# Kernel optimization log

Measured on AMD Instinct MI355X. Metric: run time of the kernel, lower is better.

The kernel has to match this reference:

```python
import jax, jax.numpy as jnp
import numpy as np

N, E, IN_D, H, OUT_D = 50000, 800000, 128, 64, 64


def setup_inputs() -> dict:
    key = jax.random.key(0)
    ks = jax.random.split(key, 16)
    s = lambda k, shape: jax.random.normal(k, shape, dtype=jnp.float32) * (1.0 / np.sqrt(shape[0]))
    return {
        "x": jax.random.normal(ks[0], (N, IN_D), dtype=jnp.float32),
        "edge_index": jax.random.randint(ks[1], (2, E), 0, N, dtype=jnp.int32),
        "W1": s(ks[2], (IN_D, H)), "b1": jnp.zeros((H,), jnp.float32),
        "W2": s(ks[3], (H, 2 * H)), "b2": jnp.zeros((2 * H,), jnp.float32),
        "W3": s(ks[4], (2 * H, 4 * H)), "b3": jnp.zeros((4 * H,), jnp.float32),
        "dec1_w": s(ks[5], (4 * H, 2 * H, 2)), "dec1_b": jnp.zeros((2 * H,), jnp.float32),
        "dec2_w": s(ks[6], (2 * H, H, 2)), "dec2_b": jnp.zeros((H,), jnp.float32),
        "dec3_w": s(ks[7], (H, H, 2)), "dec3_b": jnp.zeros((H,), jnp.float32),
        "skip1_w": s(ks[8], (2 * H, 2 * H)), "skip1_b": jnp.zeros((2 * H,), jnp.float32),
        "skip2_w": s(ks[9], (H, H)), "skip2_b": jnp.zeros((H,), jnp.float32),
        "fin_w": s(ks[10], (OUT_D, 8 * H)), "fin_b": jnp.zeros((OUT_D,), jnp.float32),
    }


def _deconv2(x, w, b):
    # ConvTranspose1d(kernel=2, stride=2): [n,c,l] x [c,o,2] -> [n,o,2l]
    y = jnp.einsum('ncl,cok->nolk', x, w)
    n, o = x.shape[0], w.shape[1]
    return y.reshape(n, o, -1) + b[None, :, None]


def reference(x, edge_index, W1, b1, W2, b2, W3, b3, dec1_w, dec1_b, dec2_w, dec2_b,
              dec3_w, dec3_b, skip1_w, skip1_b, skip2_w, skip2_b, fin_w, fin_b):
    n = x.shape[0]
    loop = jnp.arange(n, dtype=edge_index.dtype)
    src = jnp.concatenate([edge_index[0], loop])
    tgt = jnp.concatenate([edge_index[1], loop])
    deg = jax.ops.segment_sum(jnp.ones_like(src, dtype=x.dtype), tgt, num_segments=n)
    dinv = jax.lax.rsqrt(deg)  # deg >= 1 due to self-loops
    norm = dinv[src] * dinv[tgt]  # [E+N]

    def gcn(h, W, b):
        hw = h @ W
        agg = jax.ops.segment_sum(hw[src] * norm[:, None], tgt, num_segments=n)
        return agg + b

    x1 = jax.nn.gelu(gcn(x, W1, b1))    # [N, H]
    x2 = jax.nn.gelu(gcn(x1, W2, b2))   # [N, 2H]
    x3 = jax.nn.gelu(gcn(x2, W3, b3))   # [N, 4H]

    d = _deconv2(x3[:, :, None], dec1_w, dec1_b)           # [N, 2H, 2]
    d = d + (x2 @ skip1_w.T + skip1_b)[:, :, None]
    d = _deconv2(d, dec2_w, dec2_b)                        # [N, H, 4]
    d = d + (x1 @ skip2_w.T + skip2_b)[:, :, None]
    d = _deconv2(d, dec3_w, dec3_b)                        # [N, H, 8]
    out = d.reshape(n, -1) @ fin_w.T + fin_b               # [N, OUT_D]
    return out
```

## Files before the change

### kernel.cpp

```cpp
#include <hip/hip_runtime.h>
#include <hip/hip_bf16.h>

typedef __attribute__((ext_vector_type(8))) short short8_t;
typedef __attribute__((ext_vector_type(4))) float f32x4;

#define CAP 64

__device__ __forceinline__ float gelu_f(float x) {
    float x3 = x * x * x;
    return 0.5f * x * (1.0f + tanhf(0.7978845608028654f * (x + 0.044715f * x3)));
}
__device__ __forceinline__ float b2f(unsigned short u) {
    union { float f; unsigned int i; } c; c.i = ((unsigned int)u) << 16; return c.f;
}
__device__ __forceinline__ unsigned short f2bu(float f) {
    union { float f; unsigned int i; } c; c.f = f;
    unsigned int r = c.i + 0x7fffu + ((c.i >> 16) & 1u);
    return (unsigned short)(r >> 16);
}


__device__ __forceinline__ void d_EF(int bid, int t, const float* __restrict__ dec3_w,
                                     const float* __restrict__ fin_w, float* __restrict__ EF) {
    int i2 = bid * 4 + (t >> 6), od = t & 63;
    int c3 = i2 >> 2, pp = i2 & 3;
    const float* d3 = dec3_w + c3 * 128;
    const float* fw = fin_w + od * 512;
    float s = 0.f;
    #pragma unroll
    for (int o3 = 0; o3 < 64; ++o3) {
        s += d3[o3 * 2 + 0] * fw[o3 * 8 + pp * 2 + 0];
        s += d3[o3 * 2 + 1] * fw[o3 * 8 + pp * 2 + 1];
    }
    EF[i2 * 64 + od] = s;
}

__device__ __forceinline__ void d_CEF(int bid, int t, const float* __restrict__ dec2_w,
                                      const float* __restrict__ EF, float* __restrict__ CEF) {
    int i1 = bid * 4 + (t >> 6), od = t & 63;
    int c2 = i1 >> 1, lp = i1 & 1;
    const float* d2 = dec2_w + c2 * 128;
    float s = 0.f;
    #pragma unroll
    for (int o2 = 0; o2 < 64; ++o2) {
        s += d2[o2 * 2 + 0] * EF[(o2 * 4 + lp * 2 + 0) * 64 + od];
        s += d2[o2 * 2 + 1] * EF[(o2 * 4 + lp * 2 + 1) * 64 + od];
    }
    CEF[i1 * 64 + od] = s;
}

__device__ __forceinline__ void d_comp(int sb, int od,
                       const float* __restrict__ dec1_w, const float* __restrict__ skip1_w,
                       const float* __restrict__ skip2_w,
                       const float* __restrict__ dec1_b, const float* __restrict__ skip1_b,
                       const float* __restrict__ dec2_b, const float* __restrict__ skip2_b,
                       const float* __restrict__ dec3_b, const float* __restrict__ fin_w,
                       const float* __restrict__ fin_b,
                       const float* __restrict__ CEF, const float* __restrict__ EF,
                       unsigned short* __restrict__ McatT, float* __restrict__ m0) {
    if (sb < 256) {
        const float* d1 = dec1_w + sb * 256;
        float s = 0.f;
        for (int j = 0; j < 256; ++j) s += d1[j] * CEF[j * 64 + od];
        McatT[od * 448 + sb] = f2bu(s);
    } else if (sb < 384) {
        int c = sb - 256;
        float s = 0.f;
        for (int j = 0; j < 256; ++j) s += skip1_w[(j >> 1) * 128 + c] * CEF[j * 64 + od];
        McatT[od * 448 + sb] = f2bu(s);
    } else if (sb < 448) {
        int c = sb - 384;
        float s = 0.f;
        for (int j = 0; j < 256; ++j) s += skip2_w[(j >> 2) * 64 + c] * EF[j * 64 + od];
        McatT[od * 448 + sb] = f2bu(s);
    } else {
        float s = fin_b[od];
        for (int j = 0; j < 256; ++j) s += (dec1_b[j >> 1] + skip1_b[j >> 1]) * CEF[j * 64 + od];
        for (int j = 0; j < 256; ++j) s += (dec2_b[j >> 2] + skip2_b[j >> 2]) * EF[j * 64 + od];
        for (int j = 0; j < 512; ++j) s += dec3_b[j >> 3] * fin_w[od * 512 + j];
        m0[od] = s;
    }
}

__device__ __forceinline__ void d_wconv(int bid, int t,
                        const float* __restrict__ W1, const float* __restrict__ W2,
                        const float* __restrict__ W3,
                        unsigned short* __restrict__ W1T, unsigned short* __restrict__ W2T,
                        unsigned short* __restrict__ W3T) {
    int i = bid * 256 + t;
    if (i < 8192) {
        int k = i >> 6, n = i & 63;
        W1T[n * 128 + k] = f2bu(W1[i]);
    } else if (i < 16384) {
        int j = i - 8192; int k = j >> 7, n = j & 127;
        W2T[n * 64 + k] = f2bu(W2[j]);
    } else if (i < 49152) {
        int j = i - 16384; int k = j >> 8, n = j & 255;
        W3T[n * 128 + k] = f2bu(W3[j]);
    }
}

__device__ __forceinline__ void d_fillx(int bid, int t, const int* __restrict__ src,
                                        const int* __restrict__ tgt, int E,
                                        int* __restrict__ cnt, unsigned short* __restrict__ csru) {
    int i = (bid * 256 + t) * 8;
    if (i + 7 < E) {
        int4 t0 = *(const int4*)(tgt + i);
        int4 t1 = *(const int4*)(tgt + i + 4);
        int4 s0 = *(const int4*)(src + i);
        int4 s1 = *(const int4*)(src + i + 4);
        int k0 = atomicAdd(&cnt[t0.x], 1);
        int k1 = atomicAdd(&cnt[t0.y], 1);
        int k2 = atomicAdd(&cnt[t0.z], 1);
        int k3 = atomicAdd(&cnt[t0.w], 1);
        int k4 = atomicAdd(&cnt[t1.x], 1);
        int k5 = atomicAdd(&cnt[t1.y], 1);
        int k6 = atomicAdd(&cnt[t1.z], 1);
        int k7 = atomicAdd(&cnt[t1.w], 1);
        if (k0 < CAP - 1) csru[(t0.x << 6) + k0] = (unsigned short)s0.x;
        if (k1 < CAP - 1) csru[(t0.y << 6) + k1] = (unsigned short)s0.y;
        if (k2 < CAP - 1) csru[(t0.z << 6) + k2] = (unsigned short)s0.z;
        if (k3 < CAP - 1) csru[(t0.w << 6) + k3] = (unsigned short)s0.w;
        if (k4 < CAP - 1) csru[(t1.x << 6) + k4] = (unsigned short)s1.x;
        if (k5 < CAP - 1) csru[(t1.y << 6) + k5] = (unsigned short)s1.y;
        if (k6 < CAP - 1) csru[(t1.z << 6) + k6] = (unsigned short)s1.z;
        if (k7 < CAP - 1) csru[(t1.w << 6) + k7] = (unsigned short)s1.w;
    } else {
        for (int k = i; k < E; ++k) {
            int tt = tgt[k];
            int kk = atomicAdd(&cnt[tt], 1);
            if (kk < CAP - 1) csru[(tt << 6) + kk] = (unsigned short)src[k];
        }
    }
}

template<bool A32, bool BIAS, bool GELU, bool OUT32>
__device__ __forceinline__ void d_gmm(
    int bx, int by,
    const unsigned short* __restrict__ A, const float* __restrict__ Af, int lda,
    const unsigned short* __restrict__ Bt, int ldb,
    const float* __restrict__ bias,
    void* __restrict__ Cv, int ldc, int M, int K) {
    constexpr int LDS_R = 72;
    __shared__ unsigned short As[64 * LDS_R];
    __shared__ unsigned short Bs[64 * LDS_R];
    const int tid = threadIdx.x;
    const int r0 = bx * 64, c0 = by * 64;
    const int w = tid >> 6, lane = tid & 63;
    const int wm = (w >> 1) * 32, wn = (w & 1) * 32;
    const int fr = lane & 15, kg = lane >> 4;
    f32x4 acc[2][2];
    #pragma unroll
    for (int m = 0; m < 2; ++m)
        #pragma unroll
        for (int n = 0; n < 2; ++n) { f32x4 z = {0.f, 0.f, 0.f, 0.f}; acc[m][n] = z; }

    const int sr = tid >> 2, sc = (tid & 3) * 16;
    const bool aok = (r0 + sr) < M;
    const unsigned short* ag = A32 ? nullptr : (A + (size_t)(r0 + sr) * lda + sc);
    const float* agf = A32 ? (Af + (size_t)(r0 + sr) * lda + sc) : nullptr;
    const unsigned short* bg = Bt + (size_t)(c0 + sr) * ldb + sc;

    for (int kt = 0; kt < K; kt += 64) {
        if (aok) {
            if constexpr (A32) {
                float4 f0 = *(const float4*)(agf + kt);
                float4 f1 = *(const float4*)(agf + kt + 4);
                float4 f2 = *(const float4*)(agf + kt + 8);
                float4 f3 = *(const float4*)(agf + kt + 12);
                unsigned short o[16] = { f2bu(f0.x), f2bu(f0.y), f2bu(f0.z), f2bu(f0.w),
                                         f2bu(f1.x), f2bu(f1.y), f2bu(f1.z), f2bu(f1.w),
                                         f2bu(f2.x), f2bu(f2.y), f2bu(f2.z), f2bu(f2.w),
                                         f2bu(f3.x), f2bu(f3.y), f2bu(f3.z), f2bu(f3.w) };
                *(uint4*)&As[sr * LDS_R + sc]     = ((const uint4*)o)[0];
                *(uint4*)&As[sr * LDS_R + sc + 8] = ((const uint4*)o)[1];
            } else {
                *(uint4*)&As[sr * LDS_R + sc]     = *(const uint4*)(ag + kt);
                *(uint4*)&As[sr * LDS_R + sc + 8] = *(const uint4*)(ag + kt + 8);
            }
        }
        *(uint4*)&Bs[sr * LDS_R + sc]     = *(const uint4*)(bg + kt);
        *(uint4*)&Bs[sr * LDS_R + sc + 8] = *(const uint4*)(bg + kt + 8);
        __syncthreads();
        #pragma unroll
        for (int s2 = 0; s2 < 2; ++s2) {
            short8_t afr[2], bfr[2];
            #pragma unroll
            for (int n = 0; n < 2; ++n)
                bfr[n] = *(const short8_t*)&Bs[(wn + n * 16 + fr) * LDS_R + s2 * 32 + kg * 8];
            #pragma unroll
            for (int m = 0; m < 2; ++m)
                afr[m] = *(const short8_t*)&As[(wm + m * 16 + fr) * LDS_R + s2 * 32 + kg * 8];
            #pragma unroll
            for (int m = 0; m < 2; ++m)
                #pragma unroll
                for (int n = 0; n < 2; ++n)
                    acc[m][n] = __builtin_amdgcn_mfma_f32_16x16x32_bf16(afr[m], bfr[n], acc[m][n], 0, 0, 0);
        }
        __syncthreads();
    }
    #pragma unroll
    for (int m = 0; m < 2; ++m) {
        #pragma unroll
        for (int n = 0; n < 2; ++n) {
            #pragma unroll
            for (int j = 0; j < 4; ++j) {
                int row = r0 + wm + m * 16 + kg * 4 + j;
                int col = c0 + wn + n * 16 + fr;
                if (row < M) {
                    float xv = acc[m][n][j];
                    if (BIAS) xv += bias[col];
                    if (GELU) xv = gelu_f(xv);
                    if (OUT32) ((float*)Cv)[(size_t)row * ldc + col] = xv;
                    else ((unsigned short*)Cv)[(size_t)row * ldc + col] = f2bu(xv);
                }
            }
        }
    }
}

template<int F, int LPN, int NN, bool FIRST, bool EPI>
__device__ __forceinline__ void d_aggb(
    int bid,
    const unsigned short* __restrict__ g, int ldi,
    const int* __restrict__ cnt, const unsigned short* __restrict__ csru,
    unsigned int* __restrict__ csrw,
    const float* __restrict__ bias,
    unsigned short* __restrict__ out, int ldo, int N) {
    constexpr int SLOTS = 64 / LPN;
    constexpr int NB = 24 / SLOTS;
    static_assert(F / LPN == 8, "V must be 8");
    __shared__ int   sIdx[4][NN][CAP];
    __shared__ float sW[4][NN][CAP];
    int tid = threadIdx.x;
    int lane = tid & 63, wv = tid >> 6;
    int vb = bid * (4 * NN) + wv * NN;
    int slot = lane / LPN, fl = lane % LPN;
    int fo = fl * 8;
    bool ok[NN];
    int vc[NN], degc[NN];
    #pragma unroll
    for (int n = 0; n < NN; ++n) {
        int v = vb + n;
        ok[n] = v < N;
        vc[n] = ok[n] ? v : 0;
    }
    #pragma unroll
    for (int n = 0; n < NN; ++n) {
        int ua; float ww;
        if constexpr (FIRST) {
            int deg = cnt[vc[n]];
            degc[n] = min(deg, CAP - 2);
            float dv = rsqrtf((float)(deg + 1));
            if (lane < degc[n])       { ua = csru[(vc[n] << 6) + lane]; ww = rsqrtf((float)(cnt[ua] + 1)) * dv; }
            else if (lane == degc[n]) { ua = vc[n]; ww = dv * dv; }
            else if (lane == 63)      { ua = degc[n]; ww = 0.f; }
            else                      { ua = vc[n]; ww = 0.f; }
            if (ok[n]) csrw[(vc[n] << 6) + lane] = ((unsigned int)f2bu(ww) << 16) | (unsigned int)ua;
        } else {
            unsigned int pa = csrw[(vc[n] << 6) + lane];
            ua = (int)(pa & 0xFFFFu);
            ww = b2f((unsigned short)(pa >> 16));
            degc[n] = (int)(csrw[(vc[n] << 6) + 63] & 0xFFFFu);
        }
        sIdx[wv][n][lane] = ua;
        sW[wv][n][lane] = ww;
    }
    int cmax = 0;
    #pragma unroll
    for (int n = 0; n < NN; ++n) cmax = max(cmax, ok[n] ? degc[n] + 1 : 0);
    float acc[NN][8] = {};
    const unsigned short* hbase = g + fo;

    uint4 tt[NN][NB];
    float wg[NN][NB];
    #pragma unroll
    for (int b = 0; b < NB; ++b) {
        int j = slot + b * SLOTS;
        #pragma unroll
        for (int n = 0; n < NN; ++n) {
            int u = sIdx[wv][n][j];
            wg[n][b] = sW[wv][n][j];
            tt[n][b] = *(const uint4*)(hbase + (size_t)u * ldi);
        }
    }
    #pragma unroll
    for (int b = 0; b < NB; ++b)
        #pragma unroll
        for (int n = 0; n < NN; ++n) {
            const unsigned short* pp = (const unsigned short*)&tt[n][b];
            #pragma unroll
            for (int q = 0; q < 8; ++q)
                acc[n][q] = fmaf(b2f(pp[q]), wg[n][b], acc[n][q]);
        }
    for (int j = NB * SLOTS + slot; j < cmax; j += SLOTS) {
        #pragma unroll
        for (int n = 0; n < NN; ++n) {
            int u = sIdx[wv][n][j];
            float w = sW[wv][n][j];
            uint4 t = *(const uint4*)(hbase + (size_t)u * ldi);
            const unsigned short* pp = (const unsigned short*)&t;
            #pragma unroll
            for (int q = 0; q < 8; ++q)
                acc[n][q] = fmaf(b2f(pp[q]), w, acc[n][q]);
        }
    }
    #pragma unroll
    for (int off = LPN; off < 64; off <<= 1)
        #pragma unroll
        for (int n = 0; n < NN; ++n)
            #pragma unroll
            for (int q = 0; q < 8; ++q)
                acc[n][q] += __shfl_xor(acc[n][q], off, 64);
    if (slot == 0) {
        #pragma unroll
        for (int n = 0; n < NN; ++n) {
            unsigned short o[8];
            #pragma unroll
            for (int q = 0; q < 8; ++q) {
                float xv = acc[n][q];
                if (EPI) xv = gelu_f(xv + bias[fo + q]);
                o[q] = f2bu(xv);
            }
            if (ok[n]) *(uint4*)(out + (size_t)(vb + n) * ldo + fo) = *(const uint4*)o;
        }
    }
}


template<bool A32, bool BIAS, bool GELU, bool OUT32>
__global__ __launch_bounds__(256) void k_gmm(
    const unsigned short* __restrict__ A, const float* __restrict__ Af, int lda,
    const unsigned short* __restrict__ Bt, int ldb,
    const float* __restrict__ bias,
    void* __restrict__ Cv, int ldc, int M, int K) {
    d_gmm<A32, BIAS, GELU, OUT32>(blockIdx.x, blockIdx.y, A, Af, lda, Bt, ldb, bias,
                                  Cv, ldc, M, K);
}

template<int F, int LPN, int NN, bool EPI>
__global__ __launch_bounds__(256) void k_aggb(
    const unsigned short* __restrict__ g, int ldi,
    unsigned int* __restrict__ csrw,
    const float* __restrict__ bias,
    unsigned short* __restrict__ out, int ldo, int N) {
    d_aggb<F, LPN, NN, false, EPI>(blockIdx.x, g, ldi, nullptr, nullptr, csrw, bias, out, ldo, N);
}

__global__ __launch_bounds__(256) void k_mega0(
    const float* __restrict__ W1, const float* __restrict__ W2, const float* __restrict__ W3,
    unsigned short* __restrict__ W1T, unsigned short* __restrict__ W2T,
    unsigned short* __restrict__ W3T,
    const float* __restrict__ dec3_w, const float* __restrict__ fin_w, float* __restrict__ EF,
    int* __restrict__ cnt, int N) {
    int b = blockIdx.x, t = threadIdx.x;
    if (b < 192) d_wconv(b, t, W1, W2, W3, W1T, W2T, W3T);
    else if (b < 256) d_EF(b - 192, t, dec3_w, fin_w, EF);
    else { int i = (b - 256) * 256 + t; if (i < N) cnt[i] = 0; }
}

__global__ __launch_bounds__(256) void k_megaA(
    const int* __restrict__ src, const int* __restrict__ tgt, int E,
    int* __restrict__ cnt, unsigned short* __restrict__ csru, int nf,
    const float* __restrict__ x, const unsigned short* __restrict__ W1T,
    unsigned short* __restrict__ hw1, int M, int ng,
    const float* __restrict__ dec2_w, const float* __restrict__ EF, float* __restrict__ CEF) {
    int b = blockIdx.x;
    if (b < nf)
        d_fillx(b, threadIdx.x, src, tgt, E, cnt, csru);
    else if (b < nf + ng)
        d_gmm<true, false, false, false>(b - nf, 0, nullptr, x, 128, W1T, 128,
                                         (const float*)nullptr, hw1, 64, M, 128);
    else
        d_CEF(b - nf - ng, threadIdx.x, dec2_w, EF, CEF);
}

__global__ __launch_bounds__(256) void k_megaB(
    const unsigned short* __restrict__ hw1,
    const int* __restrict__ cnt, const unsigned short* __restrict__ csru,
    unsigned int* __restrict__ csrw,
    const float* __restrict__ b1, unsigned short* __restrict__ x1out, int N, int na,
    const float* __restrict__ dec1_w, const float* __restrict__ skip1_w,
    const float* __restrict__ skip2_w,
    const float* __restrict__ dec1_b, const float* __restrict__ skip1_b,
    const float* __restrict__ dec2_b, const float* __restrict__ skip2_b,
    const float* __restrict__ dec3_b, const float* __restrict__ fin_w,
    const float* __restrict__ fin_b,
    const float* __restrict__ CEF, const float* __restrict__ EF,
    unsigned short* __restrict__ McatT, float* __restrict__ m0) {
    int b = blockIdx.x, t = threadIdx.x;
    if (b < na) {
        d_aggb<64, 8, 4, true, true>(b, hw1, 64, cnt, csru, csrw, b1, x1out, 448, N);
    } else {
        int sb = (b - na) * 4 + (t >> 6);
        if (sb <= 448)
            d_comp(sb, t & 63, dec1_w, skip1_w, skip2_w, dec1_b, skip1_b, dec2_b, skip2_b,
                   dec3_b, fin_w, fin_b, CEF, EF, McatT, m0);
    }
}

extern "C" void kernel_launch(void* const* d_in, const int* in_sizes, int n_in,
                              void* d_out, int out_size, void* d_ws, size_t ws_size,
                              hipStream_t stream) {
    const float* x       = (const float*)d_in[0];
    const int*   ei      = (const int*)d_in[1];
    const float* W1      = (const float*)d_in[2];
    const float* b1      = (const float*)d_in[3];
    const float* W2      = (const float*)d_in[4];
    const float* b2      = (const float*)d_in[5];
    const float* W3      = (const float*)d_in[6];
    const float* b3      = (const float*)d_in[7];
    const float* dec1_w  = (const float*)d_in[8];
    const float* dec1_b  = (const float*)d_in[9];
    const float* dec2_w  = (const float*)d_in[10];
    const float* dec2_b  = (const float*)d_in[11];
    const float* dec3_w  = (const float*)d_in[12];
    const float* dec3_b  = (const float*)d_in[13];
    const float* skip1_w = (const float*)d_in[14];
    const float* skip1_b = (const float*)d_in[15];
    const float* skip2_w = (const float*)d_in[16];
    const float* skip2_b = (const float*)d_in[17];
    const float* fin_w   = (const float*)d_in[18];
    const float* fin_b   = (const float*)d_in[19];

    const int N = in_sizes[0] / 128;
    const int E = in_sizes[1] / 2;
    const int* e_src = ei;
    const int* e_tgt = ei + E;

    char* p = (char*)d_ws;
    auto alloc = [&](size_t bytes) -> void* {
        void* r = p;
        p += (bytes + 255) & ~(size_t)255;
        return r;
    };
    int*            cnt   = (int*)alloc((size_t)N * 4);
    unsigned short* csru  = (unsigned short*)alloc((size_t)N * CAP * 2);
    unsigned int*   csrw  = (unsigned int*)alloc((size_t)N * CAP * 4);
    float* EF      = (float*)alloc(256 * 64 * 4);
    float* CEF     = (float*)alloc(256 * 64 * 4);
    float* m0      = (float*)alloc(64 * 4);
    unsigned short* McatT = (unsigned short*)alloc(64 * 448 * 2);
    unsigned short* W1T   = (unsigned short*)alloc(64 * 128 * 2);
    unsigned short* W2T   = (unsigned short*)alloc(128 * 64 * 2);
    unsigned short* W3T   = (unsigned short*)alloc(256 * 128 * 2);
    unsigned short* hw1   = (unsigned short*)alloc((size_t)N * 64 * 2);
    unsigned short* a1    = (unsigned short*)alloc((size_t)N * 64 * 2);
    unsigned short* xcat  = (unsigned short*)alloc((size_t)N * 448 * 2);
    unsigned short* a2    = hw1;
    if ((size_t)(p - (char*)d_ws) > ws_size) return;

    const int nf = (E / 8 + 255) / 256;
    const int mg = (N + 63) / 64;
    const int ag4 = (N + 15) / 16;
    const int ag2 = (N + 7) / 8;
    const int compb = (449 + 3) / 4;
    const int zb = (N + 255) / 256;

    k_mega0<<<dim3(192 + 64 + zb), dim3(256), 0, stream>>>(
        W1, W2, W3, W1T, W2T, W3T, dec3_w, fin_w, EF, cnt, N);

    k_megaA<<<dim3(nf + mg + 64), dim3(256), 0, stream>>>(
        e_src, e_tgt, E, cnt, csru, nf, x, W1T, hw1, N, mg, dec2_w, EF, CEF);

    k_megaB<<<dim3(ag4 + compb), dim3(256), 0, stream>>>(
        hw1, cnt, csru, csrw, b1, xcat + 384, N, ag4,
        dec1_w, skip1_w, skip2_w, dec1_b, skip1_b, dec2_b, skip2_b, dec3_b,
        fin_w, fin_b, CEF, EF, McatT, m0);

    k_aggb<64, 8, 4, false><<<dim3(ag4), dim3(256), 0, stream>>>(
        xcat + 384, 448, csrw, (const float*)nullptr, a1, 64, N);
    k_gmm<false, true, true, false><<<dim3(mg, 2), dim3(256), 0, stream>>>(
        a1, nullptr, 64, W2T, 64, b2, xcat + 256, 448, N, 64);

    k_aggb<128, 16, 2, false><<<dim3(ag2), dim3(256), 0, stream>>>(
        xcat + 256, 448, csrw, (const float*)nullptr, a2, 128, N);
    k_gmm<false, true, true, false><<<dim3(mg, 4), dim3(256), 0, stream>>>(
        a2, nullptr, 128, W3T, 128, b3, xcat, 448, N, 128);

    k_gmm<false, true, false, true><<<dim3(mg, 1), dim3(256), 0, stream>>>(
        xcat, nullptr, 448, McatT, 448, m0, d_out, 64, N, 448);
}
```

Baseline: 202.7 us.

## Split 64-wide gather features into two 32-column halves for better locality

The first-layer GEMM now writes hw1 as two separate N×32 bf16 half-arrays, and the layer-1 aggregation also writes x1 into two half-arrays alongside xcat. A new aggregation routine gathers each half in a separate pass with 8-lane, 8-byte loads and 2 nodes per wave. The goal is a smaller random-gather working set per pass (3.2 MB per half), so more of it stays in cache, and x1 no longer has to be gathered from the strided 448-wide xcat. The cost is extra writes for the duplicated x1, a second set of buffers, twice as many blocks, and a GEMM epilogue that does scalar stores with a branch.

```diff
diff --git a/kernel.cpp b/kernel.cpp
--- a/kernel.cpp
+++ b/kernel.cpp
@@ -134,13 +134,14 @@
     }
 }
 
-template<bool A32, bool BIAS, bool GELU, bool OUT32>
+template<bool A32, bool BIAS, bool GELU, bool OUT32, bool OUTH>
 __device__ __forceinline__ void d_gmm(
     int bx, int by,
     const unsigned short* __restrict__ A, const float* __restrict__ Af, int lda,
     const unsigned short* __restrict__ Bt, int ldb,
     const float* __restrict__ bias,
-    void* __restrict__ Cv, int ldc, int M, int K) {
+    void* __restrict__ Cv, int ldc, int M, int K,
+    unsigned short* __restrict__ ho0, unsigned short* __restrict__ ho1) {
     constexpr int LDS_R = 72;
     __shared__ unsigned short As[64 * LDS_R];
     __shared__ unsigned short Bs[64 * LDS_R];
@@ -211,8 +212,14 @@
                     float xv = acc[m][n][j];
                     if (BIAS) xv += bias[col];
                     if (GELU) xv = gelu_f(xv);
-                    if (OUT32) ((float*)Cv)[(size_t)row * ldc + col] = xv;
-                    else ((unsigned short*)Cv)[(size_t)row * ldc + col] = f2bu(xv);
+                    if (OUTH) {
+                        if (col < 32) ho0[(size_t)row * 32 + col] = f2bu(xv);
+                        else          ho1[(size_t)row * 32 + col - 32] = f2bu(xv);
+                    } else if (OUT32) {
+                        ((float*)Cv)[(size_t)row * ldc + col] = xv;
+                    } else {
+                        ((unsigned short*)Cv)[(size_t)row * ldc + col] = f2bu(xv);
+                    }
                 }
             }
         }
@@ -327,6 +334,164 @@
     }
 }
 
+template<bool FIRST, bool EPI, bool HOUT>
+__device__ __forceinline__ void d_aggbH(
+    int bid,
+    const unsigned short* __restrict__ ga, const unsigned short* __restrict__ gb,
+    const int* __restrict__ cnt, const unsigned short* __restrict__ csru,
+    unsigned int* __restrict__ csrw,
+    const float* __restrict__ bias,
+    unsigned short* __restrict__ out, int ldo,
+    unsigned short* __restrict__ oh0, unsigned short* __restrict__ oh1,
+    int N) {
+    constexpr int LPN = 8, SLOTS = 8, NB = 3, NN = 2;
+    __shared__ int   sIdx[4][NN][CAP];
+    __shared__ float sW[4][NN][CAP];
+    int tid = threadIdx.x;
+    int lane = tid & 63, wv = tid >> 6;
+    int vb = bid * (4 * NN) + wv * NN;
+    int slot = lane / LPN, fl = lane % LPN;
+    int fo = fl * 4;
+    bool ok[NN];
+    int vc[NN], degc[NN];
+    #pragma unroll
+    for (int n = 0; n < NN; ++n) {
+        int v = vb + n;
+        ok[n] = v < N;
+        vc[n] = ok[n] ? v : 0;
+    }
+    #pragma unroll
+    for (int n = 0; n < NN; ++n) {
+        int ua; float ww;
+        if constexpr (FIRST) {
+            int deg = cnt[vc[n]];
+            degc[n] = min(deg, CAP - 2);
+            float dv = rsqrtf((float)(deg + 1));
+            if (lane < degc[n])       { ua = csru[(vc[n] << 6) + lane]; ww = rsqrtf((float)(cnt[ua] + 1)) * dv; }
+            else if (lane == degc[n]) { ua = vc[n]; ww = dv * dv; }
+            else if (lane == 63)      { ua = degc[n]; ww = 0.f; }
+            else                      { ua = vc[n]; ww = 0.f; }
+            if (ok[n]) csrw[(vc[n] << 6) + lane] = ((unsigned int)f2bu(ww) << 16) | (unsigned int)ua;
+        } else {
+            unsigned int pa = csrw[(vc[n] << 6) + lane];
+            ua = (int)(pa & 0xFFFFu);
+            ww = b2f((unsigned short)(pa >> 16));
+            degc[n] = (int)(csrw[(vc[n] << 6) + 63] & 0xFFFFu);
+        }
+        sIdx[wv][n][lane] = ua;
+        sW[wv][n][lane] = ww;
+    }
+    int cmax = 0;
+    #pragma unroll
+    for (int n = 0; n < NN; ++n) cmax = max(cmax, ok[n] ? degc[n] + 1 : 0);
+    float accA[NN][4] = {}, accB[NN][4] = {};
+
+    {
+        uint2 ta[NN][NB];
+        float wA[NN][NB];
+        #pragma unroll
+        for (int b = 0; b < NB; ++b) {
+            int j = slot + b * SLOTS;
+            #pragma unroll
+            for (int n = 0; n < NN; ++n) {
+                int u = sIdx[wv][n][j];
+                wA[n][b] = sW[wv][n][j];
+                ta[n][b] = *(const uint2*)(ga + (size_t)u * 32 + fo);
+            }
+        }
+        #pragma unroll
+        for (int b = 0; b < NB; ++b)
+            #pragma unroll
+            for (int n = 0; n < NN; ++n) {
+                const unsigned short* pp = (const unsigned short*)&ta[n][b];
+                #pragma unroll
+                for (int q = 0; q < 4; ++q)
+                    accA[n][q] = fmaf(b2f(pp[q]), wA[n][b], accA[n][q]);
+            }
+        for (int j = NB * SLOTS + slot; j < cmax; j += SLOTS) {
+            #pragma unroll
+            for (int n = 0; n < NN; ++n) {
+                int u = sIdx[wv][n][j];
+                float w = sW[wv][n][j];
+                uint2 t = *(const uint2*)(ga + (size_t)u * 32 + fo);
+                const unsigned short* pp = (const unsigned short*)&t;
+                #pragma unroll
+                for (int q = 0; q < 4; ++q)
+                    accA[n][q] = fmaf(b2f(pp[q]), w, accA[n][q]);
+            }
+        }
+    }
+    {
+        uint2 tb[NN][NB];
+        float wB[NN][NB];
+        #pragma unroll
+        for (int b = 0; b < NB; ++b) {
+            int j = slot + b * SLOTS;
+            #pragma unroll
+            for (int n = 0; n < NN; ++n) {
+                int u = sIdx[wv][n][j];
+                wB[n][b] = sW[wv][n][j];
+                tb[n][b] = *(const uint2*)(gb + (size_t)u * 32 + fo);
+            }
+        }
+        #pragma unroll
+        for (int b = 0; b < NB; ++b)
+            #pragma unroll
+            for (int n = 0; n < NN; ++n) {
+                const unsigned short* pp = (const unsigned short*)&tb[n][b];
+                #pragma unroll
+                for (int q = 0; q < 4; ++q)
+                    accB[n][q] = fmaf(b2f(pp[q]), wB[n][b], accB[n][q]);
+            }
+        for (int j = NB * SLOTS + slot; j < cmax; j += SLOTS) {
+            #pragma unroll
+            for (int n = 0; n < NN; ++n) {
+                int u = sIdx[wv][n][j];
+                float w = sW[wv][n][j];
+                uint2 t = *(const uint2*)(gb + (size_t)u * 32 + fo);
+                const unsigned short* pp = (const unsigned short*)&t;
+                #pragma unroll
+                for (int q = 0; q < 4; ++q)
+                    accB[n][q] = fmaf(b2f(pp[q]), w, accB[n][q]);
+            }
+        }
+    }
+    #pragma unroll
+    for (int off = LPN; off < 64; off <<= 1)
+        #pragma unroll
+        for (int n = 0; n < NN; ++n)
+            #pragma unroll
+            for (int q = 0; q < 4; ++q) {
+                accA[n][q] += __shfl_xor(accA[n][q], off, 64);
+                accB[n][q] += __shfl_xor(accB[n][q], off, 64);
+            }
+    if (slot == 0) {
+        #pragma unroll
+        for (int n = 0; n < NN; ++n) {
+            unsigned short oA[4], oB[4];
+            #pragma unroll
+            for (int q = 0; q < 4; ++q) {
+                float xa = accA[n][q], xb = accB[n][q];
+                if (EPI) {
+                    xa = gelu_f(xa + bias[fo + q]);
+                    xb = gelu_f(xb + bias[32 + fo + q]);
+                }
+                oA[q] = f2bu(xa);
+                oB[q] = f2bu(xb);
+            }
+            if (ok[n]) {
+                size_t row = (size_t)(vb + n);
+                *(uint2*)(out + row * ldo + fo)      = *(const uint2*)oA;
+                *(uint2*)(out + row * ldo + 32 + fo) = *(const uint2*)oB;
+                if (HOUT) {
+                    *(uint2*)(oh0 + row * 32 + fo) = *(const uint2*)oA;
+                    *(uint2*)(oh1 + row * 32 + fo) = *(const uint2*)oB;
+                }
+            }
+        }
+    }
+}
+
 
 template<bool A32, bool BIAS, bool GELU, bool OUT32>
 __global__ __launch_bounds__(256) void k_gmm(
@@ -334,8 +499,8 @@
     const unsigned short* __restrict__ Bt, int ldb,
     const float* __restrict__ bias,
     void* __restrict__ Cv, int ldc, int M, int K) {
-    d_gmm<A32, BIAS, GELU, OUT32>(blockIdx.x, blockIdx.y, A, Af, lda, Bt, ldb, bias,
-                                  Cv, ldc, M, K);
+    d_gmm<A32, BIAS, GELU, OUT32, false>(blockIdx.x, blockIdx.y, A, Af, lda, Bt, ldb, bias,
+                                         Cv, ldc, M, K, nullptr, nullptr);
 }
 
 template<int F, int LPN, int NN, bool EPI>
@@ -345,6 +510,14 @@
     const float* __restrict__ bias,
     unsigned short* __restrict__ out, int ldo, int N) {
     d_aggb<F, LPN, NN, false, EPI>(blockIdx.x, g, ldi, nullptr, nullptr, csrw, bias, out, ldo, N);
+}
+
+__global__ __launch_bounds__(256) void k_aggbH2(
+    const unsigned short* __restrict__ x1a, const unsigned short* __restrict__ x1b,
+    unsigned int* __restrict__ csrw,
+    unsigned short* __restrict__ a1, int N) {
+    d_aggbH<false, false, false>(blockIdx.x, x1a, x1b, nullptr, nullptr, csrw,
+                                 (const float*)nullptr, a1, 64, nullptr, nullptr, N);
 }
 
 __global__ __launch_bounds__(256) void k_mega0(
@@ -363,23 +536,25 @@
     const int* __restrict__ src, const int* __restrict__ tgt, int E,
     int* __restrict__ cnt, unsigned short* __restrict__ csru, int nf,
     const float* __restrict__ x, const unsigned short* __restrict__ W1T,
-    unsigned short* __restrict__ hw1, int M, int ng,
+    unsigned short* __restrict__ hw1a, unsigned short* __restrict__ hw1b, int M, int ng,
     const float* __restrict__ dec2_w, const float* __restrict__ EF, float* __restrict__ CEF) {
     int b = blockIdx.x;
     if (b < nf)
         d_fillx(b, threadIdx.x, src, tgt, E, cnt, csru);
     else if (b < nf + ng)
-        d_gmm<true, false, false, false>(b - nf, 0, nullptr, x, 128, W1T, 128,
-                                         (const float*)nullptr, hw1, 64, M, 128);
+        d_gmm<true, false, false, false, true>(b - nf, 0, nullptr, x, 128, W1T, 128,
+                                               (const float*)nullptr, nullptr, 0, M, 128,
+                                               hw1a, hw1b);
     else
         d_CEF(b - nf - ng, threadIdx.x, dec2_w, EF, CEF);
 }
 
 __global__ __launch_bounds__(256) void k_megaB(
-    const unsigned short* __restrict__ hw1,
+    const unsigned short* __restrict__ hw1a, const unsigned short* __restrict__ hw1b,
     const int* __restrict__ cnt, const unsigned short* __restrict__ csru,
     unsigned int* __restrict__ csrw,
-    const float* __restrict__ b1, unsigned short* __restrict__ x1out, int N, int na,
+    const float* __restrict__ b1, unsigned short* __restrict__ x1out,
+    unsigned short* __restrict__ x1a, unsigned short* __restrict__ x1b, int N, int na,
     const float* __restrict__ dec1_w, const float* __restrict__ skip1_w,
     const float* __restrict__ skip2_w,
     const float* __restrict__ dec1_b, const float* __restrict__ skip1_b,
@@ -390,7 +565,8 @@
     unsigned short* __restrict__ McatT, float* __restrict__ m0) {
     int b = blockIdx.x, t = threadIdx.x;
     if (b < na) {
-        d_aggb<64, 8, 4, true, true>(b, hw1, 64, cnt, csru, csrw, b1, x1out, 448, N);
+        d_aggbH<true, true, true>(b, hw1a, hw1b, cnt, csru, csrw, b1,
+                                  x1out, 448, x1a, x1b, N);
     } else {
         int sb = (b - na) * 4 + (t >> 6);
         if (sb <= 448)
@@ -444,15 +620,17 @@
     unsigned short* W1T   = (unsigned short*)alloc(64 * 128 * 2);
     unsigned short* W2T   = (unsigned short*)alloc(128 * 64 * 2);
     unsigned short* W3T   = (unsigned short*)alloc(256 * 128 * 2);
-    unsigned short* hw1   = (unsigned short*)alloc((size_t)N * 64 * 2);
+    unsigned short* hw1a  = (unsigned short*)alloc((size_t)N * 32 * 2);
+    unsigned short* hw1b  = (unsigned short*)alloc((size_t)N * 32 * 2);
+    unsigned short* x1a   = (unsigned short*)alloc((size_t)N * 32 * 2);
+    unsigned short* x1b   = (unsigned short*)alloc((size_t)N * 32 * 2);
     unsigned short* a1    = (unsigned short*)alloc((size_t)N * 64 * 2);
+    unsigned short* a2    = (unsigned short*)alloc((size_t)N * 128 * 2);
     unsigned short* xcat  = (unsigned short*)alloc((size_t)N * 448 * 2);
-    unsigned short* a2    = hw1;
     if ((size_t)(p - (char*)d_ws) > ws_size) return;
 
     const int nf = (E / 8 + 255) / 256;
     const int mg = (N + 63) / 64;
-    const int ag4 = (N + 15) / 16;
     const int ag2 = (N + 7) / 8;
     const int compb = (449 + 3) / 4;
     const int zb = (N + 255) / 256;
@@ -461,15 +639,14 @@
         W1, W2, W3, W1T, W2T, W3T, dec3_w, fin_w, EF, cnt, N);
 
     k_megaA<<<dim3(nf + mg + 64), dim3(256), 0, stream>>>(
-        e_src, e_tgt, E, cnt, csru, nf, x, W1T, hw1, N, mg, dec2_w, EF, CEF);
-
-    k_megaB<<<dim3(ag4 + compb), dim3(256), 0, stream>>>(
-        hw1, cnt, csru, csrw, b1, xcat + 384, N, ag4,
+        e_src, e_tgt, E, cnt, csru, nf, x, W1T, hw1a, hw1b, N, mg, dec2_w, EF, CEF);
+
+    k_megaB<<<dim3(ag2 + compb), dim3(256), 0, stream>>>(
+        hw1a, hw1b, cnt, csru, csrw, b1, xcat + 384, x1a, x1b, N, ag2,
         dec1_w, skip1_w, skip2_w, dec1_b, skip1_b, dec2_b, skip2_b, dec3_b,
         fin_w, fin_b, CEF, EF, McatT, m0);
 
-    k_aggb<64, 8, 4, false><<<dim3(ag4), dim3(256), 0, stream>>>(
-        xcat + 384, 448, csrw, (const float*)nullptr, a1, 64, N);
+    k_aggbH2<<<dim3(ag2), dim3(256), 0, stream>>>(x1a, x1b, csrw, a1, N);
     k_gmm<false, true, true, false><<<dim3(mg, 2), dim3(256), 0, stream>>>(
         a1, nullptr, 64, W2T, 64, b2, xcat + 256, 448, N, 64);
 
```

Result: slower. 209.1 us (+3.2%).
